# Optimization experiments

Hardware: AMD Instinct MI355X
Metric: run time of the kernel (lower is better)

The kernel has to match this reference:

```python
import jax, jax.numpy as jnp
import numpy as np

NUM_LAYERS = 6
D_MODEL = 768
N_HEADS = 8
D_QKV = D_MODEL // N_HEADS
D_FF = 3072
OUT_DIM = 80
MAX_REL = 100  # relative_positional_distance
NUM_REL = 2 * MAX_REL + 1
LN_EPS = 1e-5


def layer_norm(x, g, b):
    mu = jnp.mean(x, axis=-1, keepdims=True)
    var = jnp.mean((x - mu) ** 2, axis=-1, keepdims=True)
    return (x - mu) / jnp.sqrt(var + LN_EPS) * g + b


def rel_positional_logits(q, emb):
    # q: (B,H,L,dq) (already scaled by 1/sqrt(dq)); emb: (H, 2*MAX_REL+1, dq)
    B, H, L, dq = q.shape
    pad_len = max(L - MAX_REL, 0)
    start = max(MAX_REL - L, 0)
    padded = jnp.pad(emb, ((0, 0), (pad_len, pad_len), (0, 0)))
    used = padded[:, start:start + 2 * L - 1]  # (H, 2L-1, dq)
    logits = jnp.einsum('bhld,hmd->bhlm', q, used)  # (B,H,L,2L-1)
    if L > MAX_REL:
        # mask unreachable relative positions (|rel| beyond table) with -1e8
        mask = jnp.zeros((2 * L - 1,), logits.dtype)
        mask = mask.at[:pad_len].set(-1e8).at[-pad_len:].set(-1e8)
        logits = logits + mask
    # relative -> absolute indexing (fairseq skew trick)
    x = jnp.pad(logits, ((0, 0), (0, 0), (0, 0), (0, 1)))       # (B,H,L,2L)
    x = x.reshape(B, H, L * 2 * L)
    x = jnp.pad(x, ((0, 0), (0, 0), (0, L - 1)))
    x = x.reshape(B, H, L + 1, 2 * L - 1)
    return x[:, :, :L, L - 1:]  # (B,H,L,L)


def self_attention(x, wq, wk, wv, wo, emb):
    # x: (T,B,D); wq/wk/wv: (H,D,dq); wo: (H,dq,D); emb: (H,NUM_REL,dq)
    q = jnp.einsum('tbf,hfa->bhta', x, wq) / (D_QKV ** 0.5)
    k = jnp.einsum('tbf,hfa->bhta', x, wk)
    v = jnp.einsum('tbf,hfa->bhta', x, wv)
    logits = jnp.einsum('bhqa,bhka->bhqk', q, k) + rel_positional_logits(q, emb)
    probs = jax.nn.softmax(logits, axis=-1)
    o = jnp.einsum('bhqk,bhka->bhqa', probs, v)
    return jnp.einsum('bhta,had->tbd', o, wo)


def forward(x, wq, wk, wv, wo, rel_emb, ff1_w, ff1_b, ff2_w, ff2_b,
            ln1_g, ln1_b, ln2_g, ln2_b, wout, bout):
    # x: (B,T,D)
    src = jnp.transpose(x, (1, 0, 2))  # (T,B,D)
    for l in range(NUM_LAYERS):
        attn = self_attention(src, wq[l], wk[l], wv[l], wo[l], rel_emb[l])
        src = layer_norm(src + attn, ln1_g[l], ln1_b[l])
        h = jax.nn.relu(src @ ff1_w[l].T + ff1_b[l])
        ff = h @ ff2_w[l].T + ff2_b[l]
        src = layer_norm(src + ff, ln2_g[l], ln2_b[l])
    out = jnp.transpose(src, (1, 0, 2))  # (B,T,D)
    return out @ wout.T + bout


def setup_inputs() -> dict:
    key = jax.random.key(0)
    ks = jax.random.split(key, 17)
    B, T = 8, 512
    s_d = 1.0 / np.sqrt(D_MODEL)
    s_q = 1.0 / np.sqrt(D_QKV)
    s_f = 1.0 / np.sqrt(D_FF)
    f32 = jnp.float32
    return {
        'x': jax.random.normal(ks[0], (B, T, D_MODEL), f32),
        'wq': jax.random.normal(ks[1], (NUM_LAYERS, N_HEADS, D_MODEL, D_QKV), f32) * s_d,
        'wk': jax.random.normal(ks[2], (NUM_LAYERS, N_HEADS, D_MODEL, D_QKV), f32) * s_d,
        'wv': jax.random.normal(ks[3], (NUM_LAYERS, N_HEADS, D_MODEL, D_QKV), f32) * s_d,
        'wo': jax.random.normal(ks[4], (NUM_LAYERS, N_HEADS, D_QKV, D_MODEL), f32) * s_q,
        'rel_emb': jax.random.normal(ks[5], (NUM_LAYERS, N_HEADS, NUM_REL, D_QKV), f32) * s_q,
        'ff1_w': jax.random.normal(ks[6], (NUM_LAYERS, D_FF, D_MODEL), f32) * s_d,
        'ff1_b': jnp.zeros((NUM_LAYERS, D_FF), f32),
        'ff2_w': jax.random.normal(ks[7], (NUM_LAYERS, D_MODEL, D_FF), f32) * s_f,
        'ff2_b': jnp.zeros((NUM_LAYERS, D_MODEL), f32),
        'ln1_g': jnp.ones((NUM_LAYERS, D_MODEL), f32),
        'ln1_b': jnp.zeros((NUM_LAYERS, D_MODEL), f32),
        'ln2_g': jnp.ones((NUM_LAYERS, D_MODEL), f32),
        'ln2_b': jnp.zeros((NUM_LAYERS, D_MODEL), f32),
        'wout': jax.random.normal(ks[8], (OUT_DIM, D_MODEL), f32) * s_d,
        'bout': jnp.zeros((OUT_DIM,), f32),
    }


def reference(x, wq, wk, wv, wo, rel_emb, ff1_w, ff1_b, ff2_w, ff2_b,
              ln1_g, ln1_b, ln2_g, ln2_b, wout, bout):
    return forward(x, wq, wk, wv, wo, rel_emb, ff1_w, ff1_b, ff2_w, ff2_b,
                   ln1_g, ln1_b, ln2_g, ln2_b, wout, bout)
```

## Files before the change

### kernel.cpp

```cpp
#include <hip/hip_runtime.h>
#include <hip/hip_bf16.h>
#include <math.h>

#define NL   6
#define DM   768
#define NH   8
#define DQ   96
#define DFF  3072
#define BB   8
#define TT   512
#define NTOK (BB*TT)
#define NREL 201
#define WIN  99
#define ODIM 80
#define NQKV 2304
#define RELD 208

typedef __attribute__((ext_vector_type(8))) short v8s;
typedef __attribute__((ext_vector_type(4))) float v4f;

static __device__ __forceinline__ short bf16bits(float x) {
  __hip_bfloat16 h = __float2bfloat16(x);
  return *(short*)&h;
}

__global__ void k_transpose_in(const float* __restrict__ x, float* __restrict__ src,
                               __hip_bfloat16* __restrict__ srcb) {
  int n = blockIdx.x;
  int t = n >> 3, b = n & 7;
  const float* xi = x + ((size_t)b*TT + t)*DM;
  for (int d = threadIdx.x; d < DM; d += blockDim.x) {
    float v = xi[d];
    src[(size_t)n*DM + d] = v;
    srcb[(size_t)n*DM + d] = __float2bfloat16(v);
  }
}

__global__ void k_conv_qkvw(const float* __restrict__ wq, const float* __restrict__ wk,
                            const float* __restrict__ wv, __hip_bfloat16* __restrict__ o) {
  size_t idx = (size_t)blockIdx.x*256 + threadIdx.x;
  if (idx >= (size_t)NL*NQKV*DM) return;
  int f = idx % DM; size_t rest = idx / DM;
  int n = rest % NQKV; int l = rest / NQKV;
  int part = n / DM, c = n % DM;
  int h = c / DQ, a = c % DQ;
  size_t si = (size_t)l*DM*DM + ((size_t)h*DM + f)*DQ + a;
  float v = (part == 0) ? wq[si]*0.10206207261596577f : (part == 1 ? wk[si] : wv[si]);
  o[idx] = __float2bfloat16(v);
}

__global__ void k_conv_wo(const float* __restrict__ wo, __hip_bfloat16* __restrict__ o) {
  size_t idx = (size_t)blockIdx.x*256 + threadIdx.x;
  if (idx >= (size_t)NL*DM*DM) return;
  int r = idx % DM; size_t rest = idx / DM;
  int d = rest % DM; int l = rest / DM;
  o[idx] = __float2bfloat16(wo[(size_t)l*DM*DM + (size_t)r*DM + d]);
}

__global__ void k_cast(const float* __restrict__ in, __hip_bfloat16* __restrict__ o, size_t n) {
  size_t idx = (size_t)blockIdx.x*256 + threadIdx.x;
  if (idx < n) o[idx] = __float2bfloat16(in[idx]);
}

__global__ void k_conv_wout(const float* __restrict__ wout, __hip_bfloat16* __restrict__ o) {
  int idx = blockIdx.x*256 + threadIdx.x;
  if (idx >= 128*DM) return;
  int n = idx / DM, f = idx % DM;
  o[idx] = __float2bfloat16(n < ODIM ? wout[(size_t)n*DM + f] : 0.f);
}

template<int BM, int BN, int WM, int WN, bool RELU, bool BF16OUT, bool PERM>
__global__ __launch_bounds__(256)
void k_mfma_gemm(const __hip_bfloat16* __restrict__ A, const __hip_bfloat16* __restrict__ Bt,
                 const float* __restrict__ bias, void* __restrict__ Cv,
                 int K, int Nvalid, int ldc) {
  constexpr int NWN = BN/WN;
  constexpr int FM = WM/16, FN = WN/16;
  __shared__ __align__(16) short As[2][BM*64];
  __shared__ __align__(16) short Bs[2][BN*64];
  const int tid = threadIdx.x;
  const int m0 = blockIdx.x*BM, n0 = blockIdx.y*BN;
  const int lane = tid & 63, w = tid >> 6;
  const int wm = (w / NWN)*WM, wn = (w % NWN)*WN;
  const int mr = lane & 15, q4 = lane >> 4;
  const short* Ag = (const short*)A;
  const short* Bg = (const short*)Bt;
  const v4f zero = {0.f, 0.f, 0.f, 0.f};
  v4f acc[FM][FN];
  #pragma unroll
  for (int i=0;i<FM;++i)
    #pragma unroll
    for (int j=0;j<FN;++j) acc[i][j] = zero;

  auto stage = [&](int k0, int buf) {
    #pragma unroll
    for (int s = 0; s < (BM*8)/256; ++s) {
      int cid = s*256 + tid;
      int row = cid >> 3;
      int c = (cid & 7) ^ (row & 7);
      __builtin_amdgcn_global_load_lds(
        (const __attribute__((address_space(1))) void*)(Ag + (size_t)(m0+row)*K + k0 + c*8),
        (__attribute__((address_space(3))) void*)(&As[buf][cid*8]), 16, 0, 0);
    }
    #pragma unroll
    for (int s = 0; s < (BN*8)/256; ++s) {
      int cid = s*256 + tid;
      int row = cid >> 3;
      int c = (cid & 7) ^ (row & 7);
      __builtin_amdgcn_global_load_lds(
        (const __attribute__((address_space(1))) void*)(Bg + (size_t)(n0+row)*K + k0 + c*8),
        (__attribute__((address_space(3))) void*)(&Bs[buf][cid*8]), 16, 0, 0);
    }
  };

  const int nk = K >> 6;
  stage(0, 0);
  for (int i = 0; i < nk; ++i) {
    __syncthreads();
    if (i + 1 < nk) stage((i+1)*64, (i+1)&1);
    const short* Ab = As[i&1];
    const short* Bb = Bs[i&1];
    #pragma unroll
    for (int kh = 0; kh < 2; ++kh) {
      int pos = (kh*4 + q4) ^ (mr & 7);
      v8s af[FM], bf[FN];
      #pragma unroll
      for (int ii=0;ii<FM;++ii) af[ii] = *(const v8s*)(Ab + (wm + ii*16 + mr)*64 + pos*8);
      #pragma unroll
      for (int j=0;j<FN;++j) bf[j] = *(const v8s*)(Bb + (wn + j*16 + mr)*64 + pos*8);
      #pragma unroll
      for (int ii=0;ii<FM;++ii)
        #pragma unroll
        for (int j=0;j<FN;++j)
          acc[ii][j] = __builtin_amdgcn_mfma_f32_16x16x32_bf16(af[ii], bf[j], acc[ii][j], 0, 0, 0);
    }
  }

  #pragma unroll
  for (int j=0;j<FN;++j) {
    int col = n0 + wn + j*16 + mr;
    if (col < Nvalid) {
      float bv = bias ? bias[col] : 0.f;
      #pragma unroll
      for (int i=0;i<FM;++i) {
        #pragma unroll
        for (int r=0;r<4;++r) {
          int m = m0 + wm + i*16 + q4*4 + r;
          float val = acc[i][j][r] + bv;
          if (RELU) val = fmaxf(val, 0.f);
          int row = PERM ? ((m & 7)*TT + (m >> 3)) : m;
          if (BF16OUT) ((__hip_bfloat16*)Cv)[(size_t)row*ldc + col] = __float2bfloat16(val);
          else         ((float*)Cv)[(size_t)row*ldc + col] = val;
        }
      }
    }
  }
}

__global__ __launch_bounds__(256)
void k_rel_gemm(const __hip_bfloat16* __restrict__ qkvb,
                const __hip_bfloat16* __restrict__ embb,
                float* __restrict__ rel) {
  const int e0 = blockIdx.x*64, m0 = blockIdx.y*64, h = blockIdx.z;
  const int tid = threadIdx.x, lane = tid & 63, w = tid >> 6;
  const int l15 = lane & 15, q4 = lane >> 4;
  __shared__ __align__(16) short As[64*104];
  __shared__ __align__(16) short Bs[64*104];
  const short* qg = (const short*)qkvb;
  const short* eg = (const short*)embb;
  {
    int row = tid >> 2;
    const short* sa = qg + (size_t)(m0+row)*NQKV + h*DQ;
    int er = e0 + row; if (er > 200) er = 200;
    const short* sb = eg + ((size_t)h*NREL + er)*DQ;
    short* da = As + row*104;
    short* db = Bs + row*104;
    #pragma unroll
    for (int c = 0; c < 3; ++c) {
      int ch = (tid & 3)*3 + c;
      *(v8s*)(da + ch*8) = *(const v8s*)(sa + ch*8);
      *(v8s*)(db + ch*8) = *(const v8s*)(sb + ch*8);
    }
  }
  __syncthreads();
  const v4f zero = {0.f,0.f,0.f,0.f};
  v4f acc[4] = {zero, zero, zero, zero};
  #pragma unroll
  for (int ks = 0; ks < 3; ++ks) {
    v8s af = *(const v8s*)(As + (w*16 + l15)*104 + ks*32 + q4*8);
    #pragma unroll
    for (int f = 0; f < 4; ++f) {
      v8s bf = *(const v8s*)(Bs + (f*16 + l15)*104 + ks*32 + q4*8);
      acc[f] = __builtin_amdgcn_mfma_f32_16x16x32_bf16(af, bf, acc[f], 0, 0, 0);
    }
  }
  #pragma unroll
  for (int f = 0; f < 4; ++f) {
    int e = e0 + f*16 + l15;
    if (e < 2*WIN + 1) {
      #pragma unroll
      for (int r = 0; r < 4; ++r) {
        int n = m0 + w*16 + q4*4 + r;
        rel[((size_t)h*NTOK + n)*RELD + e] = acc[f][r];
      }
    }
  }
}

__global__ __launch_bounds__(256)
void k_attn_mfma(const __hip_bfloat16* __restrict__ qkvb,
                 const float* __restrict__ rel,
                 __hip_bfloat16* __restrict__ o) {
  const int qt = blockIdx.x, h = blockIdx.y, b = blockIdx.z;
  const int qlo = qt*64;
  const int tid = threadIdx.x, lane = tid & 63, w = tid >> 6;
  const int l15 = lane & 15, q4 = lane >> 4;
  __shared__ __align__(16) short Qs[64*104];
  __shared__ __align__(16) short Ks[64*104];
  __shared__ __align__(16) short Vt[96*72];
  __shared__ __align__(16) short Ps[64*72];
  const short* qg = (const short*)qkvb;

  {
    int row = tid >> 2;
    const short* src = qg + (size_t)((qlo+row)*8 + b)*NQKV + h*DQ;
    short* dst = Qs + row*104;
    #pragma unroll
    for (int c = 0; c < 3; ++c) {
      int ch = (tid & 3)*3 + c;
      *(v8s*)(dst + ch*8) = *(const v8s*)(src + ch*8);
    }
  }

  v4f sacc[5][4];
  const v4f neg = {-1e30f,-1e30f,-1e30f,-1e30f};
  #pragma unroll
  for (int kt=0;kt<5;++kt)
    #pragma unroll
    for (int f=0;f<4;++f) sacc[kt][f] = neg;

  const int i_row0 = qlo + w*16 + q4*4;

  for (int kt = 0; kt < 5; ++kt) {
    int kt0 = qlo + kt*64 - 128;
    if (kt0 + 64 <= 0 || kt0 >= TT) continue;
    {
      int row = tid >> 2;
      int j = kt0 + row; j = j < 0 ? 0 : (j > TT-1 ? TT-1 : j);
      const short* src = qg + (size_t)(j*8 + b)*NQKV + DM + h*DQ;
      short* dst = Ks + row*104;
      #pragma unroll
      for (int c = 0; c < 3; ++c) {
        int ch = (tid & 3)*3 + c;
        *(v8s*)(dst + ch*8) = *(const v8s*)(src + ch*8);
      }
    }
    __syncthreads();
    #pragma unroll
    for (int f = 0; f < 4; ++f) {
      int j = kt0 + f*16 + l15;
      #pragma unroll
      for (int r = 0; r < 4; ++r) {
        int i = i_row0 + r;
        int d = j - i;
        float val = -1e30f;
        if (j >= 0 && j < TT && d >= -WIN && d <= WIN)
          val = rel[((size_t)h*NTOK + i*8 + b)*RELD + d + WIN];
        sacc[kt][f][r] = val;
      }
    }
    #pragma unroll
    for (int ks = 0; ks < 3; ++ks) {
      v8s af = *(const v8s*)(Qs + (w*16 + l15)*104 + ks*32 + q4*8);
      #pragma unroll
      for (int f = 0; f < 4; ++f) {
        v8s bf = *(const v8s*)(Ks + (f*16 + l15)*104 + ks*32 + q4*8);
        sacc[kt][f] = __builtin_amdgcn_mfma_f32_16x16x32_bf16(af, bf, sacc[kt][f], 0, 0, 0);
      }
    }
    __syncthreads();
  }

  float inv[4];
  #pragma unroll
  for (int r = 0; r < 4; ++r) {
    float m = -1e30f;
    #pragma unroll
    for (int kt=0;kt<5;++kt)
      #pragma unroll
      for (int f=0;f<4;++f) m = fmaxf(m, sacc[kt][f][r]);
    #pragma unroll
    for (int off=1; off<16; off<<=1) m = fmaxf(m, __shfl_xor(m, off));
    float l = 0.f;
    #pragma unroll
    for (int kt=0;kt<5;++kt)
      #pragma unroll
      for (int f=0;f<4;++f) {
        float p = __expf(sacc[kt][f][r] - m);
        sacc[kt][f][r] = p; l += p;
      }
    #pragma unroll
    for (int off=1; off<16; off<<=1) l += __shfl_xor(l, off);
    inv[r] = 1.f / l;
  }

  v4f oacc[6];
  const v4f zero = {0.f,0.f,0.f,0.f};
  #pragma unroll
  for (int f=0;f<6;++f) oacc[f] = zero;
  for (int kt = 0; kt < 5; ++kt) {
    int kt0 = qlo + kt*64 - 128;
    if (kt0 + 64 <= 0 || kt0 >= TT) continue;
    #pragma unroll
    for (int f=0;f<4;++f)
      #pragma unroll
      for (int r=0;r<4;++r)
        Ps[(w*16 + q4*4 + r)*72 + f*16 + l15] = bf16bits(sacc[kt][f][r]);
    {
      int j = kt0 + (tid >> 2);
      int jc = j < 0 ? 0 : (j > TT-1 ? TT-1 : j);
      const short* src = qg + (size_t)(jc*8 + b)*NQKV + 2*DM + h*DQ + (tid & 3)*24;
      union { v8s v[3]; short s[24]; } u;
      u.v[0] = *(const v8s*)(src);
      u.v[1] = *(const v8s*)(src + 8);
      u.v[2] = *(const v8s*)(src + 16);
      int a0 = (tid & 3)*24, jl = tid >> 2;
      #pragma unroll
      for (int t=0;t<24;++t) Vt[(a0+t)*72 + jl] = u.s[t];
    }
    __syncthreads();
    #pragma unroll
    for (int ks=0;ks<2;++ks) {
      v8s af = *(const v8s*)(Ps + (w*16 + l15)*72 + ks*32 + q4*8);
      #pragma unroll
      for (int f=0;f<6;++f) {
        v8s bf = *(const v8s*)(Vt + (f*16 + l15)*72 + ks*32 + q4*8);
        oacc[f] = __builtin_amdgcn_mfma_f32_16x16x32_bf16(af, bf, oacc[f], 0, 0, 0);
      }
    }
    __syncthreads();
  }

  #pragma unroll
  for (int f=0;f<6;++f)
    #pragma unroll
    for (int r=0;r<4;++r) {
      int i = i_row0 + r;
      o[(size_t)(i*8 + b)*DM + h*DQ + f*16 + l15] = __float2bfloat16(oacc[f][r] * inv[r]);
    }
}

__global__ __launch_bounds__(256)
void k_ln_residual(float* __restrict__ src, const float* __restrict__ res,
                   const float* __restrict__ g, const float* __restrict__ bta,
                   __hip_bfloat16* __restrict__ srcb) {
  __shared__ float red[4];
  int n = blockIdx.x;
  float x[3];
  float s = 0.f;
  #pragma unroll
  for (int u=0;u<3;++u) {
    int d = u*256 + threadIdx.x;
    x[u] = src[(size_t)n*DM + d] + res[(size_t)n*DM + d];
    s += x[u];
  }
  #pragma unroll
  for (int off=32; off; off>>=1) s += __shfl_xor(s, off);
  if ((threadIdx.x & 63) == 0) red[threadIdx.x>>6] = s;
  __syncthreads();
  float mu = (red[0]+red[1]+red[2]+red[3]) * (1.f/DM);
  __syncthreads();
  float vs = 0.f;
  #pragma unroll
  for (int u=0;u<3;++u) { float dv = x[u]-mu; vs += dv*dv; }
  #pragma unroll
  for (int off=32; off; off>>=1) vs += __shfl_xor(vs, off);
  if ((threadIdx.x & 63) == 0) red[threadIdx.x>>6] = vs;
  __syncthreads();
  float rstd = rsqrtf((red[0]+red[1]+red[2]+red[3])*(1.f/DM) + 1e-5f);
  #pragma unroll
  for (int u=0;u<3;++u) {
    int d = u*256 + threadIdx.x;
    float v = (x[u]-mu)*rstd*g[d] + bta[d];
    src[(size_t)n*DM + d] = v;
    srcb[(size_t)n*DM + d] = __float2bfloat16(v);
  }
}

extern "C" void kernel_launch(void* const* d_in, const int* in_sizes, int n_in,
                              void* d_out, int out_size, void* d_ws, size_t ws_size,
                              hipStream_t stream) {
  const float* x    = (const float*)d_in[0];
  const float* wq   = (const float*)d_in[1];
  const float* wk   = (const float*)d_in[2];
  const float* wv   = (const float*)d_in[3];
  const float* wo   = (const float*)d_in[4];
  const float* remb = (const float*)d_in[5];
  const float* ff1w = (const float*)d_in[6];
  const float* ff1b = (const float*)d_in[7];
  const float* ff2w = (const float*)d_in[8];
  const float* ff2b = (const float*)d_in[9];
  const float* ln1g = (const float*)d_in[10];
  const float* ln1b = (const float*)d_in[11];
  const float* ln2g = (const float*)d_in[12];
  const float* ln2b = (const float*)d_in[13];
  const float* wout = (const float*)d_in[14];
  const float* bout = (const float*)d_in[15];
  float* out = (float*)d_out;

  float* wsp = (float*)d_ws;
  size_t off = 0;
  float* src  = wsp + off;                              off += (size_t)NTOK*DM;
  __hip_bfloat16* srcb  = (__hip_bfloat16*)(wsp + off); off += (size_t)NTOK*DM/2;
  __hip_bfloat16* qkvb  = (__hip_bfloat16*)(wsp + off); off += (size_t)NTOK*NQKV/2;
  float* rel  = wsp + off;                              off += (size_t)NH*NTOK*RELD;
  float* tmp  = wsp + off;                              off += (size_t)NTOK*DM;
  __hip_bfloat16* qkvwbA = (__hip_bfloat16*)(wsp + off); off += (size_t)NL*NQKV*DM/2;
  __hip_bfloat16* wobA   = (__hip_bfloat16*)(wsp + off); off += (size_t)NL*DM*DM/2;
  __hip_bfloat16* ff1wbA = (__hip_bfloat16*)(wsp + off); off += (size_t)NL*DFF*DM/2;
  __hip_bfloat16* ff2wbA = (__hip_bfloat16*)(wsp + off); off += (size_t)NL*DM*DFF/2;
  __hip_bfloat16* woutb  = (__hip_bfloat16*)(wsp + off); off += (size_t)128*DM/2;
  __hip_bfloat16* embbA  = (__hip_bfloat16*)(wsp + off); off += (size_t)NL*NH*NREL*DQ/2 + 64;
  __hip_bfloat16* hb  = (__hip_bfloat16*)qkvb;
  __hip_bfloat16* obb = srcb;
  (void)off; (void)ws_size; (void)in_sizes; (void)n_in; (void)out_size;

  dim3 b256(256);

  k_conv_qkvw<<<dim3(((size_t)NL*NQKV*DM+255)/256), b256, 0, stream>>>(wq, wk, wv, qkvwbA);
  k_conv_wo<<<dim3(((size_t)NL*DM*DM+255)/256), b256, 0, stream>>>(wo, wobA);
  k_cast<<<dim3(((size_t)NL*DFF*DM+255)/256), b256, 0, stream>>>(ff1w, ff1wbA, (size_t)NL*DFF*DM);
  k_cast<<<dim3(((size_t)NL*DM*DFF+255)/256), b256, 0, stream>>>(ff2w, ff2wbA, (size_t)NL*DM*DFF);
  k_cast<<<dim3(((size_t)NL*NH*NREL*DQ+255)/256), b256, 0, stream>>>(remb, embbA, (size_t)NL*NH*NREL*DQ);
  k_conv_wout<<<dim3((128*DM+255)/256), b256, 0, stream>>>(wout, woutb);

  k_transpose_in<<<dim3(NTOK), b256, 0, stream>>>(x, src, srcb);

  for (int l = 0; l < NL; ++l) {
    __hip_bfloat16* qkvwb = qkvwbA + (size_t)l*NQKV*DM;
    __hip_bfloat16* wob   = wobA   + (size_t)l*DM*DM;
    __hip_bfloat16* ff1wb = ff1wbA + (size_t)l*DFF*DM;
    __hip_bfloat16* ff2wb = ff2wbA + (size_t)l*DM*DFF;
    __hip_bfloat16* embb  = embbA  + (size_t)l*NH*NREL*DQ;

    k_mfma_gemm<64,128,64,32,false,true,false><<<dim3(NTOK/64, NQKV/128), b256, 0, stream>>>(
        srcb, qkvwb, nullptr, qkvb, DM, NQKV, NQKV);

    k_rel_gemm<<<dim3(4, NTOK/64, NH), b256, 0, stream>>>(qkvb, embb, rel);

    k_attn_mfma<<<dim3(TT/64, NH, BB), b256, 0, stream>>>(qkvb, rel, obb);

    k_mfma_gemm<64,64,32,32,false,false,false><<<dim3(NTOK/64, DM/64), b256, 0, stream>>>(
        obb, wob, nullptr, tmp, DM, DM, DM);
    k_ln_residual<<<dim3(NTOK), b256, 0, stream>>>(src, tmp, ln1g + (size_t)l*DM, ln1b + (size_t)l*DM, srcb);

    k_mfma_gemm<64,128,64,32,true,true,false><<<dim3(NTOK/64, DFF/128), b256, 0, stream>>>(
        srcb, ff1wb, ff1b + (size_t)l*DFF, hb, DM, DFF, DFF);
    k_mfma_gemm<64,64,32,32,false,false,false><<<dim3(NTOK/64, DM/64), b256, 0, stream>>>(
        hb, ff2wb, ff2b + (size_t)l*DM, tmp, DFF, DM, DM);
    k_ln_residual<<<dim3(NTOK), b256, 0, stream>>>(src, tmp, ln2g + (size_t)l*DM, ln2b + (size_t)l*DM, srcb);
  }

  k_mfma_gemm<64,128,64,32,false,false,true><<<dim3(NTOK/64, 1), b256, 0, stream>>>(
      srcb, woutb, bout, out, DM, ODIM, ODIM);
}
```

Baseline: 1.305 ms.

## Use 128x128 single-buffered GEMM tiles and tiled transposes for weight conversion

Adds a DBUF template flag to the MFMA GEMM so it can run single-buffered, and switches the QKV and FF1 projections to 128x128 tiles with 64x64 warp tiles and single buffering. The larger tiles raise operand reuse per LDS load, and single buffering keeps the LDS footprint down. The weight-conversion kernels for QKV and output-projection weights now transpose through a shared-memory tile, giving coalesced reads and writes instead of strided gathers. Single buffering gives up the overlap of global loads with compute, and the larger tiles launch fewer blocks.

```diff
diff --git a/kernel.cpp b/kernel.cpp
--- a/kernel.cpp
+++ b/kernel.cpp
@@ -23,6 +23,10 @@
   __hip_bfloat16 h = __float2bfloat16(x);
   return *(short*)&h;
 }
+static __device__ __forceinline__ unsigned short bf16u(float x) {
+  __hip_bfloat16 h = __float2bfloat16(x);
+  return *(unsigned short*)&h;
+}
 
 __global__ void k_transpose_in(const float* __restrict__ x, float* __restrict__ src,
                                __hip_bfloat16* __restrict__ srcb) {
@@ -36,25 +40,54 @@
   }
 }
 
-__global__ void k_conv_qkvw(const float* __restrict__ wq, const float* __restrict__ wk,
-                            const float* __restrict__ wv, __hip_bfloat16* __restrict__ o) {
-  size_t idx = (size_t)blockIdx.x*256 + threadIdx.x;
-  if (idx >= (size_t)NL*NQKV*DM) return;
-  int f = idx % DM; size_t rest = idx / DM;
-  int n = rest % NQKV; int l = rest / NQKV;
-  int part = n / DM, c = n % DM;
-  int h = c / DQ, a = c % DQ;
-  size_t si = (size_t)l*DM*DM + ((size_t)h*DM + f)*DQ + a;
-  float v = (part == 0) ? wq[si]*0.10206207261596577f : (part == 1 ? wk[si] : wv[si]);
-  o[idx] = __float2bfloat16(v);
-}
-
-__global__ void k_conv_wo(const float* __restrict__ wo, __hip_bfloat16* __restrict__ o) {
-  size_t idx = (size_t)blockIdx.x*256 + threadIdx.x;
-  if (idx >= (size_t)NL*DM*DM) return;
-  int r = idx % DM; size_t rest = idx / DM;
-  int d = rest % DM; int l = rest / DM;
-  o[idx] = __float2bfloat16(wo[(size_t)l*DM*DM + (size_t)r*DM + d]);
+__global__ __launch_bounds__(256)
+void k_conv_qkvw(const float* __restrict__ wq, const float* __restrict__ wk,
+                 const float* __restrict__ wv, __hip_bfloat16* __restrict__ o) {
+  __shared__ float tile[64][33];
+  const int ft = blockIdx.x, at = blockIdx.y;
+  const int l = blockIdx.z >> 3, h = blockIdx.z & 7;
+  const int f0 = ft*64, a0 = at*32;
+  const int tx = threadIdx.x & 31, ty = threadIdx.x >> 5;
+  const float* srcs[3] = {wq, wk, wv};
+  #pragma unroll
+  for (int part = 0; part < 3; ++part) {
+    const float* s = srcs[part] + (size_t)l*DM*DM + (size_t)h*DM*DQ;
+    #pragma unroll
+    for (int p = 0; p < 8; ++p)
+      tile[ty + 8*p][tx] = s[(size_t)(f0 + ty + 8*p)*DQ + (a0 + tx)];
+    __syncthreads();
+    const float sc = (part == 0) ? 0.10206207261596577f : 1.f;
+    unsigned short* d = (unsigned short*)o + (size_t)l*NQKV*DM + (size_t)(part*DM + h*DQ)*DM;
+    #pragma unroll
+    for (int p = 0; p < 4; ++p) {
+      int a = ty + 8*p;
+      int f = 2*tx;
+      ushort2 pr = make_ushort2(bf16u(tile[f][a]*sc), bf16u(tile[f+1][a]*sc));
+      *(ushort2*)(d + (size_t)(a0 + a)*DM + f0 + f) = pr;
+    }
+    __syncthreads();
+  }
+}
+
+__global__ __launch_bounds__(256)
+void k_conv_wo(const float* __restrict__ wo, __hip_bfloat16* __restrict__ o) {
+  __shared__ float tile[64][33];
+  const int rt = blockIdx.x, dt = blockIdx.y, l = blockIdx.z;
+  const int r0 = rt*64, d0 = dt*32;
+  const int tx = threadIdx.x & 31, ty = threadIdx.x >> 5;
+  const float* s = wo + (size_t)l*DM*DM;
+  #pragma unroll
+  for (int p = 0; p < 8; ++p)
+    tile[ty + 8*p][tx] = s[(size_t)(r0 + ty + 8*p)*DM + d0 + tx];
+  __syncthreads();
+  unsigned short* d = (unsigned short*)o + (size_t)l*DM*DM;
+  #pragma unroll
+  for (int p = 0; p < 4; ++p) {
+    int dd = ty + 8*p;
+    int r = 2*tx;
+    ushort2 pr = make_ushort2(bf16u(tile[r][dd]), bf16u(tile[r+1][dd]));
+    *(ushort2*)(d + (size_t)(d0 + dd)*DM + r0 + r) = pr;
+  }
 }
 
 __global__ void k_cast(const float* __restrict__ in, __hip_bfloat16* __restrict__ o, size_t n) {
@@ -69,15 +102,16 @@
   o[idx] = __float2bfloat16(n < ODIM ? wout[(size_t)n*DM + f] : 0.f);
 }
 
-template<int BM, int BN, int WM, int WN, bool RELU, bool BF16OUT, bool PERM>
+template<int BM, int BN, int WM, int WN, bool DBUF, bool RELU, bool BF16OUT, bool PERM>
 __global__ __launch_bounds__(256)
 void k_mfma_gemm(const __hip_bfloat16* __restrict__ A, const __hip_bfloat16* __restrict__ Bt,
                  const float* __restrict__ bias, void* __restrict__ Cv,
                  int K, int Nvalid, int ldc) {
   constexpr int NWN = BN/WN;
   constexpr int FM = WM/16, FN = WN/16;
-  __shared__ __align__(16) short As[2][BM*64];
-  __shared__ __align__(16) short Bs[2][BN*64];
+  constexpr int NB = DBUF ? 2 : 1;
+  __shared__ __align__(16) short As[NB][BM*64];
+  __shared__ __align__(16) short Bs[NB][BN*64];
   const int tid = threadIdx.x;
   const int m0 = blockIdx.x*BM, n0 = blockIdx.y*BN;
   const int lane = tid & 63, w = tid >> 6;
@@ -113,13 +147,7 @@
     }
   };
 
-  const int nk = K >> 6;
-  stage(0, 0);
-  for (int i = 0; i < nk; ++i) {
-    __syncthreads();
-    if (i + 1 < nk) stage((i+1)*64, (i+1)&1);
-    const short* Ab = As[i&1];
-    const short* Bb = Bs[i&1];
+  auto compute = [&](const short* Ab, const short* Bb) {
     #pragma unroll
     for (int kh = 0; kh < 2; ++kh) {
       int pos = (kh*4 + q4) ^ (mr & 7);
@@ -133,6 +161,23 @@
         #pragma unroll
         for (int j=0;j<FN;++j)
           acc[ii][j] = __builtin_amdgcn_mfma_f32_16x16x32_bf16(af[ii], bf[j], acc[ii][j], 0, 0, 0);
+    }
+  };
+
+  const int nk = K >> 6;
+  if (DBUF) {
+    stage(0, 0);
+    for (int i = 0; i < nk; ++i) {
+      __syncthreads();
+      if (i + 1 < nk) stage((i+1)*64, (i+1)&1);
+      compute(As[i&1], Bs[i&1]);
+    }
+  } else {
+    for (int i = 0; i < nk; ++i) {
+      stage(i*64, 0);
+      __syncthreads();
+      compute(As[0], Bs[0]);
+      __syncthreads();
     }
   }
 
@@ -427,8 +472,8 @@
 
   dim3 b256(256);
 
-  k_conv_qkvw<<<dim3(((size_t)NL*NQKV*DM+255)/256), b256, 0, stream>>>(wq, wk, wv, qkvwbA);
-  k_conv_wo<<<dim3(((size_t)NL*DM*DM+255)/256), b256, 0, stream>>>(wo, wobA);
+  k_conv_qkvw<<<dim3(DM/64, DQ/32, NL*NH), b256, 0, stream>>>(wq, wk, wv, qkvwbA);
+  k_conv_wo<<<dim3(DM/64, DM/32, NL), b256, 0, stream>>>(wo, wobA);
   k_cast<<<dim3(((size_t)NL*DFF*DM+255)/256), b256, 0, stream>>>(ff1w, ff1wbA, (size_t)NL*DFF*DM);
   k_cast<<<dim3(((size_t)NL*DM*DFF+255)/256), b256, 0, stream>>>(ff2w, ff2wbA, (size_t)NL*DM*DFF);
   k_cast<<<dim3(((size_t)NL*NH*NREL*DQ+255)/256), b256, 0, stream>>>(remb, embbA, (size_t)NL*NH*NREL*DQ);
@@ -443,24 +488,24 @@
     __hip_bfloat16* ff2wb = ff2wbA + (size_t)l*DM*DFF;
     __hip_bfloat16* embb  = embbA  + (size_t)l*NH*NREL*DQ;
 
-    k_mfma_gemm<64,128,64,32,false,true,false><<<dim3(NTOK/64, NQKV/128), b256, 0, stream>>>(
+    k_mfma_gemm<128,128,64,64,false,false,true,false><<<dim3(NTOK/128, NQKV/128), b256, 0, stream>>>(
         srcb, qkvwb, nullptr, qkvb, DM, NQKV, NQKV);
 
     k_rel_gemm<<<dim3(4, NTOK/64, NH), b256, 0, stream>>>(qkvb, embb, rel);
 
     k_attn_mfma<<<dim3(TT/64, NH, BB), b256, 0, stream>>>(qkvb, rel, obb);
 
-    k_mfma_gemm<64,64,32,32,false,false,false><<<dim3(NTOK/64, DM/64), b256, 0, stream>>>(
+    k_mfma_gemm<64,64,32,32,true,false,false,false><<<dim3(NTOK/64, DM/64), b256, 0, stream>>>(
         obb, wob, nullptr, tmp, DM, DM, DM);
     k_ln_residual<<<dim3(NTOK), b256, 0, stream>>>(src, tmp, ln1g + (size_t)l*DM, ln1b + (size_t)l*DM, srcb);
 
-    k_mfma_gemm<64,128,64,32,true,true,false><<<dim3(NTOK/64, DFF/128), b256, 0, stream>>>(
+    k_mfma_gemm<128,128,64,64,false,true,true,false><<<dim3(NTOK/128, DFF/128), b256, 0, stream>>>(
         srcb, ff1wb, ff1b + (size_t)l*DFF, hb, DM, DFF, DFF);
-    k_mfma_gemm<64,64,32,32,false,false,false><<<dim3(NTOK/64, DM/64), b256, 0, stream>>>(
+    k_mfma_gemm<64,64,32,32,true,false,false,false><<<dim3(NTOK/64, DM/64), b256, 0, stream>>>(
         hb, ff2wb, ff2b + (size_t)l*DM, tmp, DFF, DM, DM);
     k_ln_residual<<<dim3(NTOK), b256, 0, stream>>>(src, tmp, ln2g + (size_t)l*DM, ln2b + (size_t)l*DM, srcb);
   }
 
-  k_mfma_gemm<64,128,64,32,false,false,true><<<dim3(NTOK/64, 1), b256, 0, stream>>>(
+  k_mfma_gemm<64,128,64,32,true,false,false,true><<<dim3(NTOK/64, 1), b256, 0, stream>>>(
       srcb, woutb, bout, out, DM, ODIM, ODIM);
 }
```

Result: faster. 1.147 ms (-12.1%).
